# Performance work log

Measured on AMD Instinct MI355X. Metric: run time of the kernel, lower is better.

The kernel has to match this reference:

```python
import jax, jax.numpy as jnp
import numpy as np


def setup_inputs() -> dict:
    key = jax.random.key(0)
    ks = jax.random.split(key, 6)
    B, N, D, E = 16, 64, 256, 256
    nodes = jax.random.normal(ks[0], (B * N, D), jnp.float32)
    edges = jax.random.normal(ks[1], (B * N * N, E), jnp.float32)
    W_in = jax.random.normal(ks[2], (2 * D + E, D), jnp.float32) / np.float32(np.sqrt(2 * D + E))
    b_in = jnp.zeros((D,), jnp.float32)
    W_coef = jax.random.normal(ks[3], (D, 1), jnp.float32) / np.float32(np.sqrt(D))
    b_coef = jnp.zeros((1,), jnp.float32)
    W_out = jax.random.normal(ks[4], (D, D), jnp.float32) / np.float32(np.sqrt(D))
    b_out = jnp.zeros((D,), jnp.float32)
    return {"nodes": nodes, "edges": edges, "W_in": W_in, "b_in": b_in,
            "W_coef": W_coef, "b_coef": b_coef, "W_out": W_out, "b_out": b_out,
            "B": B, "N": N}


def reference(nodes, edges, W_in, b_in, W_coef, b_coef, W_out, b_out, B, N):
    # Uniform nums = [N]*B special case of the ragged torch loop.
    D = nodes.shape[-1]
    n3 = nodes.reshape(B, N, D)
    # pair[b,i,j] = [node_i, node_j, edge_ij]  -> [B,N,N,2D+E]
    pair = jnp.concatenate([
        jnp.broadcast_to(n3[:, :, None, :], (B, N, N, D)),
        jnp.broadcast_to(n3[:, None, :, :], (B, N, N, D)),
        edges.reshape(B, N, N, -1),
    ], axis=-1)
    h = jax.nn.relu(pair @ W_in + b_in)            # [B,N,N,D]
    coefs = h @ W_coef + b_coef                    # [B,N,N,1]
    diag = jnp.eye(N, dtype=coefs.dtype)[None, :, :, None] * jnp.float32(1e9)
    attn = jax.nn.softmax(coefs - diag, axis=2)    # softmax over j, diag masked
    residual = jnp.sum(attn * h, axis=2)           # [B,N,D]
    new_nodes = nodes + jax.nn.relu(residual.reshape(B * N, D) @ W_out + b_out)
    return new_nodes, h.reshape(B * N * N, D)
```

## Files before the change

kernel.cpp:

```cpp
#include <hip/hip_runtime.h>
#include <hip/hip_bf16.h>

typedef unsigned int u32;
typedef unsigned short u16;
typedef __attribute__((ext_vector_type(8))) short bf16x8;
typedef __attribute__((ext_vector_type(4))) float f32x4;

#define DI __device__ __forceinline__

DI u16 f2bfu(float f){
  union{float f; u32 i;} u; u.f = f;
  u32 lsb = (u.i >> 16) & 1u;
  u.i += 0x7fffu + lsb;
  return (u16)(u.i >> 16);
}

union BU { uint4 v; bf16x8 s; };

DI void gld16(const void* g, void* l){
  __builtin_amdgcn_global_load_lds(
      (const __attribute__((address_space(1))) void*)g,
      (__attribute__((address_space(3))) void*)l, 16, 0, 0);
}

__global__ __launch_bounds__(256) void k_pack(const float* __restrict__ W_in,
                                              u16* __restrict__ Wp3,
                                              u16* __restrict__ Wp12)
{
  int idx = blockIdx.x * 256 + threadIdx.x;
  int l = idx & 63;
  int g = idx >> 6;
  int lq = l >> 4, lr = l & 15;
  u16 o[8];
  if (g < 128){
    int nt = g >> 3, kk = g & 7;
    int n  = nt * 16 + lr;
    int k0 = 512 + kk * 32 + lq * 8;
#pragma unroll
    for (int tt = 0; tt < 8; tt++) o[tt] = f2bfu(W_in[(size_t)(k0 + tt) * 256 + n]);
    *(uint4*)(Wp3 + (size_t)idx * 8) = *(uint4*)o;
  } else {
    int g2 = g - 128;
    int half = g2 >> 7, rem = g2 & 127;
    int nt = rem >> 3, kk = rem & 7;
    int n  = nt * 16 + lr;
    int k0 = half * 256 + kk * 32 + lq * 8;
#pragma unroll
    for (int tt = 0; tt < 8; tt++) o[tt] = f2bfu(W_in[(size_t)(k0 + tt) * 256 + n]);
    *(uint4*)(Wp12 + (size_t)g2 * 512 + (size_t)l * 8) = *(uint4*)o;
  }
}

__global__ __launch_bounds__(256) void k_pre(
    const float* __restrict__ nodes, const float* __restrict__ b_in,
    const u16* __restrict__ Wp12, float* __restrict__ P1, float* __restrict__ P2)
{
  const int t = threadIdx.x;
  const int w = t >> 6, l = t & 63, lq = l >> 4, lr = l & 15;
  const int bid = blockIdx.x;
  const int rt = bid >> 3, half = (bid >> 2) & 1, cg = bid & 3;

  bf16x8 af[8];
  {
    const float* ap = nodes + (size_t)(rt * 64 + 16 * w + lr) * 256 + lq * 8;
#pragma unroll
    for (int kk = 0; kk < 8; kk++){
      float4 x = *(const float4*)(ap + kk * 32);
      float4 y = *(const float4*)(ap + kk * 32 + 4);
      bf16x8 a;
      a[0]=(short)f2bfu(x.x); a[1]=(short)f2bfu(x.y); a[2]=(short)f2bfu(x.z); a[3]=(short)f2bfu(x.w);
      a[4]=(short)f2bfu(y.x); a[5]=(short)f2bfu(y.y); a[6]=(short)f2bfu(y.z); a[7]=(short)f2bfu(y.w);
      af[kk] = a;
    }
  }
  const uint4* wp = (const uint4*)(Wp12 + (size_t)half * 128 * 512);
  float* P = half ? P2 : P1;
#pragma unroll
  for (int ntl = 0; ntl < 4; ntl++){
    const int nt = cg * 4 + ntl;
    f32x4 acc = {0.f, 0.f, 0.f, 0.f};
#pragma unroll
    for (int kk = 0; kk < 8; kk++){
      BU bu; bu.v = wp[(nt * 8 + kk) * 64 + l];
      acc = __builtin_amdgcn_mfma_f32_16x16x32_bf16(af[kk], bu.s, acc, 0, 0, 0);
    }
    const int col = nt * 16 + lr;
    const float bv = half ? 0.f : b_in[col];
#pragma unroll
    for (int r = 0; r < 4; r++){
      const int row = rt * 64 + 16 * w + 4 * lq + r;
      P[(size_t)row * 256 + col] = acc[r] + bv;
    }
  }
}

__global__ __launch_bounds__(256, 3) void k_main(
    const float* __restrict__ nodes, const float* __restrict__ edges,
    const u16* __restrict__ Wp3, const float* __restrict__ W_coef,
    const float* __restrict__ b_coef, const float* __restrict__ W_out,
    const float* __restrict__ b_out, const float* __restrict__ P1,
    const float* __restrict__ P2, float* __restrict__ out_nodes,
    float* __restrict__ out_h)
{
  __shared__ uint4 wS[2][1024];
  __shared__ float coefS[64];
  __shared__ float attnS[64];
  __shared__ float resW[4][256];
  __shared__ float resS[256];

  const int t = threadIdx.x;
  const int w = t >> 6, l = t & 63, lq = l >> 4, lr = l & 15;
  const int bi = blockIdx.x;
  const int b = bi >> 6, i = bi & 63;

  const char* wp3b = (const char*)Wp3;
  auto stage = [&](int bufi, int ntc){
    const char* src = wp3b + (size_t)ntc * 16384;
    char* dst = (char*)&wS[bufi][0];
#pragma unroll
    for (int c = 0; c < 4; ++c)
      gld16(src + c * 4096 + w * 1024 + l * 16, dst + c * 4096 + w * 1024);
  };

  stage(0, 0);

  bf16x8 af[8];
  {
    const float* ap = edges + (size_t)bi * 16384 + (size_t)(16 * w + lr) * 256 + lq * 8;
#pragma unroll
    for (int kk = 0; kk < 8; kk++){
      float4 x = *(const float4*)(ap + kk * 32);
      float4 y = *(const float4*)(ap + kk * 32 + 4);
      bf16x8 a;
      a[0]=(short)f2bfu(x.x); a[1]=(short)f2bfu(x.y); a[2]=(short)f2bfu(x.z); a[3]=(short)f2bfu(x.w);
      a[4]=(short)f2bfu(y.x); a[5]=(short)f2bfu(y.y); a[6]=(short)f2bfu(y.z); a[7]=(short)f2bfu(y.w);
      af[kk] = a;
    }
  }

  const float* p1p = P1 + (size_t)bi * 256;
  const float* p2p = P2 + (size_t)b * 64 * 256;

  f32x4 acc[16];
#pragma unroll
  for (int nt = 0; nt < 16; nt++) acc[nt] = (f32x4){0.f, 0.f, 0.f, 0.f};
  float cpart[4] = {0.f, 0.f, 0.f, 0.f};

  __syncthreads();
  int buf = 0;
#pragma unroll
  for (int ntc = 0; ntc < 8; ntc++){
    if (ntc < 7) stage(buf ^ 1, ntc + 1);
#pragma unroll
    for (int nt2 = 0; nt2 < 2; nt2++){
      const int nt = ntc * 2 + nt2;
      const u16* wsb = (const u16*)&wS[buf][nt2 * 512];
#pragma unroll
      for (int kk = 0; kk < 8; kk++){
        BU bu; bu.v = *(const uint4*)(wsb + (size_t)(kk * 64 + l) * 8);
        acc[nt] = __builtin_amdgcn_mfma_f32_16x16x32_bf16(af[kk], bu.s, acc[nt], 0, 0, 0);
      }
      const int col = nt * 16 + lr;
      const float p1 = p1p[col];
      const float wc = W_coef[col];
#pragma unroll
      for (int r = 0; r < 4; r++){
        const int row = 16 * w + 4 * lq + r;
        const float p2 = p2p[row * 256 + col];
        float h = acc[nt][r] + p1 + p2;
        h = h > 0.f ? h : 0.f;
        acc[nt][r] = h;
        out_h[((size_t)bi * 64 + row) * 256 + col] = h;
        cpart[r] += h * wc;
      }
    }
    __syncthreads();
    buf ^= 1;
  }

#pragma unroll
  for (int r = 0; r < 4; r++){
    float v = cpart[r];
    v += __shfl_xor(v, 1, 64);
    v += __shfl_xor(v, 2, 64);
    v += __shfl_xor(v, 4, 64);
    v += __shfl_xor(v, 8, 64);
    if (lr == 0) coefS[16 * w + 4 * lq + r] = v;
  }
  __syncthreads();

  if (t < 64){
    int j = t;
    float val = coefS[j] + b_coef[0] - (j == i ? 1e9f : 0.f);
    float m = val;
#pragma unroll
    for (int off = 32; off >= 1; off >>= 1){ float o = __shfl_xor(m, off, 64); m = m > o ? m : o; }
    float e = __expf(val - m);
    float s = e;
#pragma unroll
    for (int off = 32; off >= 1; off >>= 1) s += __shfl_xor(s, off, 64);
    attnS[j] = e / s;
  }
  __syncthreads();

  {
    const float a0 = attnS[16 * w + 4 * lq + 0];
    const float a1 = attnS[16 * w + 4 * lq + 1];
    const float a2 = attnS[16 * w + 4 * lq + 2];
    const float a3 = attnS[16 * w + 4 * lq + 3];
#pragma unroll
    for (int nt = 0; nt < 16; nt++){
      float part = a0 * acc[nt][0] + a1 * acc[nt][1] + a2 * acc[nt][2] + a3 * acc[nt][3];
      part += __shfl_xor(part, 16, 64);
      part += __shfl_xor(part, 32, 64);
      if (lq == (nt & 3)) resW[w][nt * 16 + lr] = part;
    }
  }
  __syncthreads();
  resS[t] = resW[0][t] + resW[1][t] + resW[2][t] + resW[3][t];
  __syncthreads();

  {
    const int d = t;
    float acco = b_out[d];
#pragma unroll 8
    for (int k4 = 0; k4 < 64; k4++){
      float4 r4 = *(const float4*)&resS[k4 * 4];
      acco += r4.x * W_out[(size_t)(k4 * 4 + 0) * 256 + d];
      acco += r4.y * W_out[(size_t)(k4 * 4 + 1) * 256 + d];
      acco += r4.z * W_out[(size_t)(k4 * 4 + 2) * 256 + d];
      acco += r4.w * W_out[(size_t)(k4 * 4 + 3) * 256 + d];
    }
    float nv = nodes[(size_t)bi * 256 + d];
    out_nodes[(size_t)bi * 256 + d] = nv + (acco > 0.f ? acco : 0.f);
  }
}

extern "C" void kernel_launch(void* const* d_in, const int* in_sizes, int n_in,
                              void* d_out, int out_size, void* d_ws, size_t ws_size,
                              hipStream_t stream)
{
  const float* nodes  = (const float*)d_in[0];
  const float* edges  = (const float*)d_in[1];
  const float* W_in   = (const float*)d_in[2];
  const float* b_in   = (const float*)d_in[3];
  const float* W_coef = (const float*)d_in[4];
  const float* b_coef = (const float*)d_in[5];
  const float* W_out  = (const float*)d_in[6];
  const float* b_out  = (const float*)d_in[7];
  (void)in_sizes; (void)n_in; (void)out_size; (void)ws_size;

  float* P1  = (float*)d_ws;
  float* P2  = P1 + 262144;
  u16*  Wp3  = (u16*)(P2 + 262144);
  u16*  Wp12 = Wp3 + 65536;

  float* out_nodes = (float*)d_out;
  float* out_h = out_nodes + 262144;

  hipLaunchKernelGGL(k_pack, dim3(96),   dim3(256), 0, stream, W_in, Wp3, Wp12);
  hipLaunchKernelGGL(k_pre,  dim3(128),  dim3(256), 0, stream, nodes, b_in, Wp12, P1, P2);
  hipLaunchKernelGGL(k_main, dim3(1024), dim3(256), 0, stream,
                     nodes, edges, Wp3, W_coef, b_coef, W_out, b_out,
                     P1, P2, out_nodes, out_h);
}
```

Measured before the change: 172.4 us.

## Stream edge tiles over K with swapped MFMA operands and vectorized h stores

```diff
diff --git a/kernel.cpp b/kernel.cpp
--- a/kernel.cpp
+++ b/kernel.cpp
@@ -5,6 +5,7 @@
 typedef unsigned short u16;
 typedef __attribute__((ext_vector_type(8))) short bf16x8;
 typedef __attribute__((ext_vector_type(4))) float f32x4;
+typedef __attribute__((ext_vector_type(4))) float f4;
 
 #define DI __device__ __forceinline__
 
@@ -21,6 +22,14 @@
   __builtin_amdgcn_global_load_lds(
       (const __attribute__((address_space(1))) void*)g,
       (__attribute__((address_space(3))) void*)l, 16, 0, 0);
+}
+
+DI float redlr(float v){
+  v += __shfl_xor(v, 1, 64);
+  v += __shfl_xor(v, 2, 64);
+  v += __shfl_xor(v, 4, 64);
+  v += __shfl_xor(v, 8, 64);
+  return v;
 }
 
 __global__ __launch_bounds__(256) void k_pack(const float* __restrict__ W_in,
@@ -33,7 +42,7 @@
   int lq = l >> 4, lr = l & 15;
   u16 o[8];
   if (g < 128){
-    int nt = g >> 3, kk = g & 7;
+    int kk = g >> 4, nt = g & 15;
     int n  = nt * 16 + lr;
     int k0 = 512 + kk * 32 + lq * 8;
 #pragma unroll
@@ -112,86 +121,86 @@
   const int w = t >> 6, l = t & 63, lq = l >> 4, lr = l & 15;
   const int bi = blockIdx.x;
   const int b = bi >> 6, i = bi & 63;
+  const int j = 16 * w + lr;
 
   const char* wp3b = (const char*)Wp3;
-  auto stage = [&](int bufi, int ntc){
-    const char* src = wp3b + (size_t)ntc * 16384;
+  auto stage = [&](int bufi, int kk){
+    const char* src = wp3b + (size_t)kk * 16384;
     char* dst = (char*)&wS[bufi][0];
 #pragma unroll
-    for (int c = 0; c < 4; ++c)
-      gld16(src + c * 4096 + w * 1024 + l * 16, dst + c * 4096 + w * 1024);
+    for (int c = 0; c < 4; ++c){
+      const int ntc = w * 4 + c;
+      gld16(src + ntc * 1024 + l * 16, dst + ntc * 1024);
+    }
   };
 
+  const f4* ebase = (const f4*)(edges + (size_t)bi * 16384 + (size_t)j * 256 + lq * 8);
+  auto ldedge = [&](int kk, f4& r0, f4& r1){
+    const f4* p = ebase + kk * 8;
+    r0 = __builtin_nontemporal_load(p);
+    r1 = __builtin_nontemporal_load(p + 1);
+  };
+  auto conv = [&](f4 x, f4 y){
+    bf16x8 a;
+    a[0]=(short)f2bfu(x[0]); a[1]=(short)f2bfu(x[1]); a[2]=(short)f2bfu(x[2]); a[3]=(short)f2bfu(x[3]);
+    a[4]=(short)f2bfu(y[0]); a[5]=(short)f2bfu(y[1]); a[6]=(short)f2bfu(y[2]); a[7]=(short)f2bfu(y[3]);
+    return a;
+  };
+
+  f32x4 acc[16];
+#pragma unroll
+  for (int nt = 0; nt < 16; nt++) acc[nt] = (f32x4){0.f, 0.f, 0.f, 0.f};
+
   stage(0, 0);
-
-  bf16x8 af[8];
-  {
-    const float* ap = edges + (size_t)bi * 16384 + (size_t)(16 * w + lr) * 256 + lq * 8;
-#pragma unroll
-    for (int kk = 0; kk < 8; kk++){
-      float4 x = *(const float4*)(ap + kk * 32);
-      float4 y = *(const float4*)(ap + kk * 32 + 4);
-      bf16x8 a;
-      a[0]=(short)f2bfu(x.x); a[1]=(short)f2bfu(x.y); a[2]=(short)f2bfu(x.z); a[3]=(short)f2bfu(x.w);
-      a[4]=(short)f2bfu(y.x); a[5]=(short)f2bfu(y.y); a[6]=(short)f2bfu(y.z); a[7]=(short)f2bfu(y.w);
-      af[kk] = a;
-    }
+  f4 rc0, rc1, rn0, rn1;
+  ldedge(0, rc0, rc1);
+
+#pragma unroll
+  for (int kk = 0; kk < 8; kk++){
+    __syncthreads();
+    if (kk < 7){
+      stage((kk + 1) & 1, kk + 1);
+      ldedge(kk + 1, rn0, rn1);
+    }
+    const bf16x8 ef = conv(rc0, rc1);
+#pragma unroll
+    for (int nt = 0; nt < 16; nt++){
+      BU bu; bu.v = wS[kk & 1][nt * 64 + l];
+      acc[nt] = __builtin_amdgcn_mfma_f32_16x16x32_bf16(bu.s, ef, acc[nt], 0, 0, 0);
+    }
+    rc0 = rn0; rc1 = rn1;
   }
 
   const float* p1p = P1 + (size_t)bi * 256;
-  const float* p2p = P2 + (size_t)b * 64 * 256;
-
-  f32x4 acc[16];
-#pragma unroll
-  for (int nt = 0; nt < 16; nt++) acc[nt] = (f32x4){0.f, 0.f, 0.f, 0.f};
-  float cpart[4] = {0.f, 0.f, 0.f, 0.f};
-
-  __syncthreads();
-  int buf = 0;
-#pragma unroll
-  for (int ntc = 0; ntc < 8; ntc++){
-    if (ntc < 7) stage(buf ^ 1, ntc + 1);
-#pragma unroll
-    for (int nt2 = 0; nt2 < 2; nt2++){
-      const int nt = ntc * 2 + nt2;
-      const u16* wsb = (const u16*)&wS[buf][nt2 * 512];
-#pragma unroll
-      for (int kk = 0; kk < 8; kk++){
-        BU bu; bu.v = *(const uint4*)(wsb + (size_t)(kk * 64 + l) * 8);
-        acc[nt] = __builtin_amdgcn_mfma_f32_16x16x32_bf16(af[kk], bu.s, acc[nt], 0, 0, 0);
-      }
-      const int col = nt * 16 + lr;
-      const float p1 = p1p[col];
-      const float wc = W_coef[col];
-#pragma unroll
-      for (int r = 0; r < 4; r++){
-        const int row = 16 * w + 4 * lq + r;
-        const float p2 = p2p[row * 256 + col];
-        float h = acc[nt][r] + p1 + p2;
-        h = h > 0.f ? h : 0.f;
-        acc[nt][r] = h;
-        out_h[((size_t)bi * 64 + row) * 256 + col] = h;
-        cpart[r] += h * wc;
-      }
-    }
-    __syncthreads();
-    buf ^= 1;
-  }
-
-#pragma unroll
-  for (int r = 0; r < 4; r++){
-    float v = cpart[r];
-    v += __shfl_xor(v, 1, 64);
-    v += __shfl_xor(v, 2, 64);
-    v += __shfl_xor(v, 4, 64);
-    v += __shfl_xor(v, 8, 64);
-    if (lr == 0) coefS[16 * w + 4 * lq + r] = v;
-  }
+  const float* p2p = P2 + ((size_t)b * 64 + j) * 256;
+  float* hop = out_h + ((size_t)bi * 64 + j) * 256;
+  float cpart = 0.f;
+#pragma unroll
+  for (int nt = 0; nt < 16; nt++){
+    const int d0 = nt * 16 + 4 * lq;
+    f4 p1v = *(const f4*)(p1p + d0);
+    f4 p2v = *(const f4*)(p2p + d0);
+    f4 wcv = *(const f4*)(W_coef + d0);
+    f4 h;
+#pragma unroll
+    for (int r = 0; r < 4; r++){
+      float x = acc[nt][r] + p1v[r] + p2v[r];
+      x = x > 0.f ? x : 0.f;
+      h[r] = x;
+      acc[nt][r] = x;
+    }
+    __builtin_nontemporal_store(h, (f4*)(hop + d0));
+    cpart += h[0]*wcv[0] + h[1]*wcv[1] + h[2]*wcv[2] + h[3]*wcv[3];
+  }
+
+  cpart += __shfl_xor(cpart, 16, 64);
+  cpart += __shfl_xor(cpart, 32, 64);
+  if (lq == 0) coefS[j] = cpart;
   __syncthreads();
 
   if (t < 64){
-    int j = t;
-    float val = coefS[j] + b_coef[0] - (j == i ? 1e9f : 0.f);
+    int jj = t;
+    float val = coefS[jj] + b_coef[0] - (jj == i ? 1e9f : 0.f);
     float m = val;
 #pragma unroll
     for (int off = 32; off >= 1; off >>= 1){ float o = __shfl_xor(m, off, 64); m = m > o ? m : o; }
@@ -199,21 +208,18 @@
     float s = e;
 #pragma unroll
     for (int off = 32; off >= 1; off >>= 1) s += __shfl_xor(s, off, 64);
-    attnS[j] = e / s;
+    attnS[jj] = e / s;
   }
   __syncthreads();
 
   {
-    const float a0 = attnS[16 * w + 4 * lq + 0];
-    const float a1 = attnS[16 * w + 4 * lq + 1];
-    const float a2 = attnS[16 * w + 4 * lq + 2];
-    const float a3 = attnS[16 * w + 4 * lq + 3];
+    const float a = attnS[j];
 #pragma unroll
     for (int nt = 0; nt < 16; nt++){
-      float part = a0 * acc[nt][0] + a1 * acc[nt][1] + a2 * acc[nt][2] + a3 * acc[nt][3];
-      part += __shfl_xor(part, 16, 64);
-      part += __shfl_xor(part, 32, 64);
-      if (lq == (nt & 3)) resW[w][nt * 16 + lr] = part;
+      f4 part;
+#pragma unroll
+      for (int r = 0; r < 4; r++) part[r] = redlr(a * acc[nt][r]);
+      if (lr == 0) *(f4*)&resW[w][nt * 16 + 4 * lq] = part;
     }
   }
   __syncthreads();
```

After: 178.8 us. +3.7%, slower.
